# Kernel tuning notes

Measured on AMD Instinct MI355X. Metric: run time of the kernel, lower is better.

Reference implementation:

```python
import jax, jax.numpy as jnp
import numpy as np

N_CODEBOOKS = 4
N_EMBED = 1024
EMBED_DIM = 64
PATCH = 4
BETA = 0.25
EPS = 1e-5
USAGE_W = 0.01


def setup_inputs() -> dict:
    key = jax.random.key(0)
    k1, k2 = jax.random.split(key)
    z = jax.random.normal(k1, (8, 64, 128, 128), dtype=jnp.float32)
    # one EMA codebook per quantizer, initialized ~ randn like torch buffer
    codebooks = jax.random.normal(k2, (N_CODEBOOKS, N_EMBED, EMBED_DIM), dtype=jnp.float32)
    return {"z": z, "codebooks": codebooks}


def _usage_loss(indices, n_embed):
    # negative-entropy penalty on code usage (no gradient path: counts are ints)
    counts = jnp.bincount(indices.reshape(-1), length=n_embed).astype(jnp.float32)
    probs = (counts + EPS) / (counts.sum() + EPS * n_embed)
    entropy = -jnp.sum(probs * jnp.log(probs + EPS))
    return jnp.log(jnp.float32(n_embed)) - entropy


def _ema_quantize(residual, embedding):
    # residual: [N, C, ph, pw], embedding: [n_e, C]; eval mode (no EMA buffer update)
    N, C, ph, pw = residual.shape
    z_flat = residual.transpose(0, 2, 3, 1).reshape(-1, C)  # [M, C]
    d = (jnp.sum(z_flat ** 2, axis=1, keepdims=True)
         + jnp.sum(embedding ** 2, axis=1)
         - 2.0 * z_flat @ embedding.T)  # [M, n_e]
    idx = jnp.argmin(d, axis=1)  # [M]
    z_q = embedding[idx].reshape(N, ph, pw, C).transpose(0, 3, 1, 2)  # [N, C, ph, pw]
    loss = BETA * jnp.mean((jax.lax.stop_gradient(z_q) - residual) ** 2)
    z_q_st = residual + jax.lax.stop_gradient(z_q - residual)  # straight-through
    return z_q_st, loss, idx.reshape(N, ph, pw)


def reference(z, codebooks):
    B, C, H, W = z.shape
    h, w = H // PATCH, W // PATCH
    # b c (h ph) (w pw) -> (b h w) c ph pw
    zp = (z.reshape(B, C, h, PATCH, w, PATCH)
            .transpose(0, 2, 4, 1, 3, 5)
            .reshape(B * h * w, C, PATCH, PATCH))
    zq_acc = jnp.zeros_like(zp)
    residual = zp
    losses, all_idx = [], []
    for i in range(N_CODEBOOKS):
        zq_i, loss_i, idx_i = _ema_quantize(residual, codebooks[i])
        loss_i = loss_i + USAGE_W * _usage_loss(idx_i, N_EMBED)
        zq_acc = zq_acc + zq_i
        residual = residual - zq_i
        losses.append(loss_i)
        all_idx.append(idx_i.reshape(idx_i.shape[0], -1))  # [N, ph*pw]
    loss = jnp.stack(losses).sum()
    # (b h w) c ph pw -> b c (h ph) (w pw)
    z_q = (zq_acc.reshape(B, h, w, C, PATCH, PATCH)
                 .transpose(0, 3, 1, 4, 2, 5)
                 .reshape(B, C, H, W))
    # [N, patch_area, n_codebooks] -> [b, h, w, patch_area, n_codebooks]
    min_idx = jnp.stack(all_idx, axis=-1).reshape(B, h, w, PATCH * PATCH, N_CODEBOOKS)
    return z_q, loss, min_idx
```

## Files before the change

kernel.cpp:

```cpp
#include <hip/hip_runtime.h>
#include <math.h>

typedef __attribute__((ext_vector_type(8))) short short8;
typedef __attribute__((ext_vector_type(4))) float f32x4;

#define NCB 4
#define NE 1024
#define DIM 64
#define HW 16384
#define NPIX 131072
#define NWAVES 4096
#define MSE_DENOM 8388608.0f
#define EPSF 1e-5f
#define CHUNK_BYTES 24576
#define CHUNK_SHORTS 12288
#define NCHUNK 16

__device__ __forceinline__ unsigned short f2bf(float x) {
    unsigned u = __float_as_uint(x);
    u += 0x7fffu + ((u >> 16) & 1u);
    return (unsigned short)(u >> 16);
}
__device__ __forceinline__ float bf2f(unsigned short h) {
    return __uint_as_float(((unsigned)h) << 16);
}

__global__ __launch_bounds__(64) void rvq_norms(const float* __restrict__ cb,
                                                float* __restrict__ nrmh) {
    int code = blockIdx.x * 64 + threadIdx.x;
    const float4* row = reinterpret_cast<const float4*>(cb + (size_t)code * DIM);
    float s0 = 0.f, s1 = 0.f, s2 = 0.f, s3 = 0.f;
#pragma unroll
    for (int k = 0; k < 16; ++k) {
        float4 v = row[k];
        s0 = fmaf(v.x, v.x, s0); s1 = fmaf(v.y, v.y, s1);
        s2 = fmaf(v.z, v.z, s2); s3 = fmaf(v.w, v.w, s3);
    }
    nrmh[code] = -0.5f * ((s0 + s1) + (s2 + s3));
}

__global__ __launch_bounds__(256) void rvq_presplit(const float* __restrict__ cb,
                                                    unsigned short* __restrict__ gB) {
    int blk = blockIdx.x;
    int tid = threadIdx.x;
    int code = tid >> 2, dg = tid & 3;
    int c0 = (blk & 15) << 6;
    int i  = blk >> 4;
    const float4* s4 = reinterpret_cast<const float4*>(
        cb + ((size_t)i * NE + c0 + code) * DIM + dg * 16);
    float v[16];
    {
        float4 q;
        q = s4[0]; v[0]=q.x; v[1]=q.y; v[2]=q.z; v[3]=q.w;
        q = s4[1]; v[4]=q.x; v[5]=q.y; v[6]=q.z; v[7]=q.w;
        q = s4[2]; v[8]=q.x; v[9]=q.y; v[10]=q.z; v[11]=q.w;
        q = s4[3]; v[12]=q.x; v[13]=q.y; v[14]=q.z; v[15]=q.w;
    }
    char* outc = reinterpret_cast<char*>(gB + (size_t)blk * CHUNK_SHORTS);
    int linbase = code * 128 + dg * 32;
    int sw = (code & 7) << 4;
#pragma unroll
    for (int h = 0; h < 2; ++h) {
        short8 p1, p2, p3;
#pragma unroll
        for (int e = 0; e < 8; ++e) {
            float t = v[h * 8 + e];
            unsigned short u1 = f2bf(t); t -= bf2f(u1);
            unsigned short u2 = f2bf(t); t -= bf2f(u2);
            unsigned short u3 = f2bf(t);
            p1[e] = (short)u1; p2[e] = (short)u2; p3[e] = (short)u3;
        }
        int a = (linbase + h * 16) ^ sw;
        *reinterpret_cast<short8*>(outc + a)         = p1;
        *reinterpret_cast<short8*>(outc + 8192 + a)  = p2;
        *reinterpret_cast<short8*>(outc + 16384 + a) = p3;
    }
}

__device__ __forceinline__ void gload16(const void* gsrc, void* ldst) {
    __builtin_amdgcn_global_load_lds(
        (const __attribute__((address_space(1))) unsigned int*)gsrc,
        (__attribute__((address_space(3))) unsigned int*)ldst, 16, 0, 0);
}

__global__ __launch_bounds__(256, 2) void rvq_main(
    const float* __restrict__ z, const unsigned short* __restrict__ gB,
    const float* __restrict__ nrmh, const float* __restrict__ cb,
    float* __restrict__ out_zq, float* __restrict__ out_idx,
    unsigned* __restrict__ hist, float* __restrict__ msePartial)
{
    __shared__ uint4 sB[2][CHUNK_BYTES / 16];
    __shared__ int   sBest[4][32];

    const int tid  = threadIdx.x;
    const int lane = tid & 63;
    const int wid  = tid >> 6;
    const int col  = lane & 15;
    const int g    = lane >> 4;
    const int blockPix = blockIdx.x * 128;
    char* sBase = reinterpret_cast<char*>(sB);
    const int sw = (col & 7) << 4;

#pragma unroll
    for (int k = 0; k < 6; ++k)
        gload16(reinterpret_cast<const char*>(gB) + k * 4096 + tid * 16,
                sBase + k * 4096 + tid * 16);

    size_t zb[2];
#pragma unroll
    for (int m = 0; m < 2; ++m) {
        int pf = blockPix + wid * 32 + m * 16 + col;
        zb[m] = (size_t)(pf >> 14) * 1048576 + (size_t)(pf & 16383);
    }

    float r[2][2][8];
#pragma unroll
    for (int m = 0; m < 2; ++m)
#pragma unroll
        for (int kh = 0; kh < 2; ++kh)
#pragma unroll
            for (int e = 0; e < 8; ++e)
                r[m][kh][e] = z[zb[m] + (size_t)(kh * 32 + g * 8 + e) * HW];

    for (int i = 0; i < NCB; ++i) {
        const char* gBi = reinterpret_cast<const char*>(gB) + (size_t)i * NCHUNK * CHUNK_BYTES;
        const float* nrm_i = nrmh + i * NE;

        short8 A[3][2][2];
#pragma unroll
        for (int m = 0; m < 2; ++m)
#pragma unroll
            for (int kh = 0; kh < 2; ++kh)
#pragma unroll
                for (int e = 0; e < 8; ++e) {
                    float t = r[m][kh][e];
                    unsigned short u1 = f2bf(t); t -= bf2f(u1);
                    unsigned short u2 = f2bf(t); t -= bf2f(u2);
                    unsigned short u3 = f2bf(t);
                    A[0][m][kh][e] = (short)u1;
                    A[1][m][kh][e] = (short)u2;
                    A[2][m][kh][e] = (short)u3;
                }

        float maxv[2][4]; int maxi[2][4];
#pragma unroll
        for (int m = 0; m < 2; ++m)
#pragma unroll
            for (int rr = 0; rr < 4; ++rr) { maxv[m][rr] = -3.4e38f; maxi[m][rr] = 0; }

        for (int c = 0; c < NCHUNK; ++c) {
            __syncthreads();
            if (c < NCHUNK - 1) {
                const char* gc = gBi + (size_t)(c + 1) * CHUNK_BYTES;
                char* sbn = sBase + ((c + 1) & 1) * CHUNK_BYTES;
#pragma unroll
                for (int k = 0; k < 6; ++k)
                    gload16(gc + k * 4096 + tid * 16, sbn + k * 4096 + tid * 16);
            }
            const char* sbc = sBase + (c & 1) * CHUNK_BYTES;

#pragma unroll
            for (int sub = 0; sub < 4; ++sub) {
                const int code = (sub << 4) + col;
                float nh = nrm_i[(c << 6) + code];

                short8 B[3][2];
#pragma unroll
                for (int sb = 0; sb < 3; ++sb) {
                    B[sb][0] = *reinterpret_cast<const short8*>(
                        sbc + sb * 8192 + ((((code << 7) + (g << 4))) ^ sw));
                    B[sb][1] = *reinterpret_cast<const short8*>(
                        sbc + sb * 8192 + ((((code << 7) + 64 + (g << 4))) ^ sw));
                }

                f32x4 acc[2][3];
#pragma unroll
                for (int m = 0; m < 2; ++m)
#pragma unroll
                    for (int rr = 0; rr < 4; ++rr) {
                        acc[m][0][rr] = nh; acc[m][1][rr] = 0.f; acc[m][2][rr] = 0.f;
                    }

                __builtin_amdgcn_s_setprio(1);
#pragma unroll
                for (int sa = 0; sa < 3; ++sa) {
#pragma unroll
                    for (int kh = 0; kh < 2; ++kh)
#pragma unroll
                        for (int sb = 0; sb < 3 - sa; ++sb) {
                            acc[0][sb] = __builtin_amdgcn_mfma_f32_16x16x32_bf16(A[sa][0][kh], B[sb][kh], acc[0][sb], 0, 0, 0);
                            acc[1][sb] = __builtin_amdgcn_mfma_f32_16x16x32_bf16(A[sa][1][kh], B[sb][kh], acc[1][sb], 0, 0, 0);
                        }
                }
                __builtin_amdgcn_s_setprio(0);

#pragma unroll
                for (int m = 0; m < 2; ++m)
#pragma unroll
                    for (int rr = 0; rr < 4; ++rr) {
                        float s = (acc[m][0][rr] + acc[m][1][rr]) + acc[m][2][rr];
                        if (s > maxv[m][rr]) { maxv[m][rr] = s; maxi[m][rr] = (c << 6) + code; }
                    }
            }
        }

        if (i < NCB - 1) {
            const char* gn = reinterpret_cast<const char*>(gB)
                           + (size_t)(i + 1) * NCHUNK * CHUNK_BYTES;
#pragma unroll
            for (int k = 0; k < 6; ++k)
                gload16(gn + k * 4096 + tid * 16, sBase + k * 4096 + tid * 16);
        }

#pragma unroll
        for (int m = 0; m < 2; ++m)
#pragma unroll
            for (int rr = 0; rr < 4; ++rr) {
                float v = maxv[m][rr]; int ix = maxi[m][rr];
#pragma unroll
                for (int off = 1; off < 16; off <<= 1) {
                    float ov = __shfl_xor(v, off, 64);
                    int   oi = __shfl_xor(ix, off, 64);
                    if (ov > v || (ov == v && oi < ix)) { v = ov; ix = oi; }
                }
                maxi[m][rr] = ix;
            }
        if (col == 0) {
#pragma unroll
            for (int m = 0; m < 2; ++m)
#pragma unroll
                for (int rr = 0; rr < 4; ++rr)
                    sBest[wid][m * 16 + g * 4 + rr] = maxi[m][rr];
        }

        const float* cbi = cb + (size_t)i * NE * DIM;
        if (lane < 16) {
#pragma unroll
            for (int m = 0; m < 2; ++m) {
                int pfr = blockPix + wid * 32 + m * 16 + lane;
                int bb = pfr >> 14, yy = (pfr >> 7) & 127, xx = pfr & 127;
                int bi = sBest[wid][m * 16 + lane];
                size_t off = (size_t)bb * 65536 + (size_t)(yy >> 2) * 2048
                           + (size_t)(xx >> 2) * 64
                           + (size_t)(((yy & 3) << 2) + (xx & 3)) * 4 + (size_t)i;
                out_idx[off] = (float)bi;
                atomicAdd(&hist[i * NE + bi], 1u);
            }
        }

#pragma unroll
        for (int m = 0; m < 2; ++m) {
            const int best = sBest[wid][m * 16 + col];
            const float* er = cbi + (size_t)best * DIM;
#pragma unroll
            for (int kh = 0; kh < 2; ++kh) {
                const float4* e4 = reinterpret_cast<const float4*>(er + kh * 32 + g * 8);
                float4 q0 = e4[0], q1 = e4[1];
                r[m][kh][0] -= q0.x; r[m][kh][1] -= q0.y;
                r[m][kh][2] -= q0.z; r[m][kh][3] -= q0.w;
                r[m][kh][4] -= q1.x; r[m][kh][5] -= q1.y;
                r[m][kh][6] -= q1.z; r[m][kh][7] -= q1.w;
            }
        }

        float s = 0.f;
#pragma unroll
        for (int m = 0; m < 2; ++m)
#pragma unroll
            for (int kh = 0; kh < 2; ++kh)
#pragma unroll
                for (int e = 0; e < 8; ++e) s = fmaf(r[m][kh][e], r[m][kh][e], s);
#pragma unroll
        for (int d_ = 32; d_ > 0; d_ >>= 1) s += __shfl_down(s, d_, 64);
        if (lane == 0) msePartial[i * NWAVES + blockIdx.x * 4 + wid] = s;
    }

#pragma unroll
    for (int m = 0; m < 2; ++m)
#pragma unroll
        for (int kh = 0; kh < 2; ++kh)
#pragma unroll
            for (int e = 0; e < 8; ++e) {
                size_t o = zb[m] + (size_t)(kh * 32 + g * 8 + e) * HW;
                out_zq[o] = z[o] - r[m][kh][e];
            }
}

__global__ __launch_bounds__(1024) void rvq_finalize(
    const unsigned* __restrict__ hist, const float* __restrict__ msePartial,
    float* __restrict__ out_loss)
{
    __shared__ float red[1024];
    int t = threadIdx.x;
    float loss = 0.f;
    for (int i = 0; i < NCB; ++i) {
        float cnt = (float)hist[i * NE + t];
        float prob = (cnt + EPSF) / (131072.0f + EPSF * 1024.0f);
        red[t] = -prob * logf(prob + EPSF);
        __syncthreads();
        for (int s = 512; s > 0; s >>= 1) { if (t < s) red[t] += red[t + s]; __syncthreads(); }
        float entropy = red[0];
        __syncthreads();
        float acc = 0.f;
#pragma unroll
        for (int k = 0; k < 4; ++k) acc += msePartial[i * NWAVES + k * 1024 + t];
        red[t] = acc;
        __syncthreads();
        for (int s = 512; s > 0; s >>= 1) { if (t < s) red[t] += red[t + s]; __syncthreads(); }
        float mse_sum = red[0];
        __syncthreads();
        loss += 0.25f * (mse_sum / MSE_DENOM) + 0.01f * (logf(1024.0f) - entropy);
    }
    if (t == 0) out_loss[0] = loss;
}

extern "C" void kernel_launch(void* const* d_in, const int* in_sizes, int n_in,
                              void* d_out, int out_size, void* d_ws, size_t ws_size,
                              hipStream_t stream) {
    const float* z  = (const float*)d_in[0];
    const float* cb = (const float*)d_in[1];

    float* out      = (float*)d_out;
    float* out_zq   = out;
    float* out_loss = out + 8388608;
    float* out_idx  = out + 8388609;

    unsigned* hist        = (unsigned*)d_ws;
    float*    nrmh        = (float*)((char*)d_ws + 16384);
    float*    msePartial  = (float*)((char*)d_ws + 32768);
    unsigned short* gB    = (unsigned short*)((char*)d_ws + 163840);

    hipMemsetAsync(d_ws, 0, 16384, stream);
    rvq_norms<<<64, 64, 0, stream>>>(cb, nrmh);
    rvq_presplit<<<64, 256, 0, stream>>>(cb, gB);
    rvq_main<<<1024, 256, 0, stream>>>(z, gB, nrmh, cb, out_zq, out_idx, hist, msePartial);
    rvq_finalize<<<1, 1024, 0, stream>>>(hist, msePartial, out_loss);
}
```

Baseline: 435.0 us.

## Prefilter codes with single-bf16 pass, rescore candidates at full precision

Nearest-code search becomes two stages. A cheap single-bf16 MFMA pass finds each pixel's approximate max score, then a bound from the residual and codebook norms sets a threshold. A second bf16 pass pushes codes above that threshold into a per-wave shared-memory list, and only those candidates are rescored with the 3-way split-bf16 product. This removes most of the 6-MFMA-per-tile exact work but adds a second sweep over the codebook, ballot and atomic list building, and uncached global gathers during rescoring. Correctness depends on the error bound and on the candidate list not overflowing CAP.

```diff
diff --git a/kernel.cpp b/kernel.cpp
--- a/kernel.cpp
+++ b/kernel.cpp
@@ -12,9 +12,9 @@
 #define NWAVES 4096
 #define MSE_DENOM 8388608.0f
 #define EPSF 1e-5f
-#define CHUNK_BYTES 24576
-#define CHUNK_SHORTS 12288
-#define NCHUNK 16
+#define CH1_BYTES 16384
+#define NCH1 8
+#define CAP 1024
 
 __device__ __forceinline__ unsigned short f2bf(float x) {
     unsigned u = __float_as_uint(x);
@@ -26,7 +26,8 @@
 }
 
 __global__ __launch_bounds__(64) void rvq_norms(const float* __restrict__ cb,
-                                                float* __restrict__ nrmh) {
+                                                float* __restrict__ nrmh,
+                                                float* __restrict__ emax2) {
     int code = blockIdx.x * 64 + threadIdx.x;
     const float4* row = reinterpret_cast<const float4*>(cb + (size_t)code * DIM);
     float s0 = 0.f, s1 = 0.f, s2 = 0.f, s3 = 0.f;
@@ -36,18 +37,22 @@
         s0 = fmaf(v.x, v.x, s0); s1 = fmaf(v.y, v.y, s1);
         s2 = fmaf(v.z, v.z, s2); s3 = fmaf(v.w, v.w, s3);
     }
-    nrmh[code] = -0.5f * ((s0 + s1) + (s2 + s3));
+    float n2 = (s0 + s1) + (s2 + s3);
+    nrmh[code] = -0.5f * n2;
+    atomicMax((int*)&emax2[blockIdx.x >> 4], __float_as_int(n2));
 }
 
 __global__ __launch_bounds__(256) void rvq_presplit(const float* __restrict__ cb,
-                                                    unsigned short* __restrict__ gB) {
+                                                    unsigned short* __restrict__ gB1,
+                                                    unsigned short* __restrict__ gBf) {
     int blk = blockIdx.x;
     int tid = threadIdx.x;
-    int code = tid >> 2, dg = tid & 3;
+    int code64 = tid >> 2, dg = tid & 3;
     int c0 = (blk & 15) << 6;
     int i  = blk >> 4;
+    int C  = c0 + code64;
     const float4* s4 = reinterpret_cast<const float4*>(
-        cb + ((size_t)i * NE + c0 + code) * DIM + dg * 16);
+        cb + ((size_t)i * NE + C) * DIM + dg * 16);
     float v[16];
     {
         float4 q;
@@ -56,9 +61,9 @@
         q = s4[2]; v[8]=q.x; v[9]=q.y; v[10]=q.z; v[11]=q.w;
         q = s4[3]; v[12]=q.x; v[13]=q.y; v[14]=q.z; v[15]=q.w;
     }
-    char* outc = reinterpret_cast<char*>(gB + (size_t)blk * CHUNK_SHORTS);
-    int linbase = code * 128 + dg * 32;
-    int sw = (code & 7) << 4;
+    char* out1 = reinterpret_cast<char*>(gB1) + (size_t)i * 131072 + (size_t)C * 128;
+    char* outf = reinterpret_cast<char*>(gBf) + (size_t)i * 393216 + (size_t)C * 384;
+    int sw = (C & 7) << 4;
 #pragma unroll
     for (int h = 0; h < 2; ++h) {
         short8 p1, p2, p3;
@@ -70,10 +75,11 @@
             unsigned short u3 = f2bf(t);
             p1[e] = (short)u1; p2[e] = (short)u2; p3[e] = (short)u3;
         }
-        int a = (linbase + h * 16) ^ sw;
-        *reinterpret_cast<short8*>(outc + a)         = p1;
-        *reinterpret_cast<short8*>(outc + 8192 + a)  = p2;
-        *reinterpret_cast<short8*>(outc + 16384 + a) = p3;
+        int al = dg * 32 + h * 16;
+        *reinterpret_cast<short8*>(out1 + (al ^ sw)) = p1;
+        *reinterpret_cast<short8*>(outf + al)        = p1;
+        *reinterpret_cast<short8*>(outf + 128 + al)  = p2;
+        *reinterpret_cast<short8*>(outf + 256 + al)  = p3;
     }
 }
 
@@ -84,13 +90,18 @@
 }
 
 __global__ __launch_bounds__(256, 2) void rvq_main(
-    const float* __restrict__ z, const unsigned short* __restrict__ gB,
-    const float* __restrict__ nrmh, const float* __restrict__ cb,
+    const float* __restrict__ z, const unsigned short* __restrict__ gB1,
+    const unsigned short* __restrict__ gBf,
+    const float* __restrict__ nrmh, const float* __restrict__ emax2,
+    const float* __restrict__ cb,
     float* __restrict__ out_zq, float* __restrict__ out_idx,
     unsigned* __restrict__ hist, float* __restrict__ msePartial)
 {
-    __shared__ uint4 sB[2][CHUNK_BYTES / 16];
+    __shared__ uint4 sB[2][CH1_BYTES / 16];
     __shared__ int   sBest[4][32];
+    __shared__ float sRn[4][32];
+    __shared__ int   sList[4][CAP];
+    __shared__ int   sCnt[4];
 
     const int tid  = threadIdx.x;
     const int lane = tid & 63;
@@ -100,11 +111,12 @@
     const int blockPix = blockIdx.x * 128;
     char* sBase = reinterpret_cast<char*>(sB);
     const int sw = (col & 7) << 4;
-
-#pragma unroll
-    for (int k = 0; k < 6; ++k)
-        gload16(reinterpret_cast<const char*>(gB) + k * 4096 + tid * 16,
-                sBase + k * 4096 + tid * 16);
+    const char* gB1b = reinterpret_cast<const char*>(gB1);
+    const char* gBfb = reinterpret_cast<const char*>(gBf);
+
+#pragma unroll
+    for (int k = 0; k < 4; ++k)
+        gload16(gB1b + k * 4096 + tid * 16, sBase + k * 4096 + tid * 16);
 
     size_t zb[2];
 #pragma unroll
@@ -123,17 +135,22 @@
                 r[m][kh][e] = z[zb[m] + (size_t)(kh * 32 + g * 8 + e) * HW];
 
     for (int i = 0; i < NCB; ++i) {
-        const char* gBi = reinterpret_cast<const char*>(gB) + (size_t)i * NCHUNK * CHUNK_BYTES;
+        const char* gB1i = gB1b + (size_t)i * 131072;
+        const char* gBfi = gBfb + (size_t)i * 393216;
         const float* nrm_i = nrmh + i * NE;
+        if (lane == 0) sCnt[wid] = 0;
 
         short8 A[3][2][2];
+        float rn2[2] = {0.f, 0.f};
 #pragma unroll
         for (int m = 0; m < 2; ++m)
 #pragma unroll
             for (int kh = 0; kh < 2; ++kh)
 #pragma unroll
                 for (int e = 0; e < 8; ++e) {
-                    float t = r[m][kh][e];
+                    float t0 = r[m][kh][e];
+                    rn2[m] = fmaf(t0, t0, rn2[m]);
+                    float t = t0;
                     unsigned short u1 = f2bf(t); t -= bf2f(u1);
                     unsigned short u2 = f2bf(t); t -= bf2f(u2);
                     unsigned short u3 = f2bf(t);
@@ -141,96 +158,194 @@
                     A[1][m][kh][e] = (short)u2;
                     A[2][m][kh][e] = (short)u3;
                 }
-
-        float maxv[2][4]; int maxi[2][4];
-#pragma unroll
-        for (int m = 0; m < 2; ++m)
-#pragma unroll
-            for (int rr = 0; rr < 4; ++rr) { maxv[m][rr] = -3.4e38f; maxi[m][rr] = 0; }
-
-        for (int c = 0; c < NCHUNK; ++c) {
+#pragma unroll
+        for (int m = 0; m < 2; ++m) {
+            rn2[m] += __shfl_xor(rn2[m], 16, 64);
+            rn2[m] += __shfl_xor(rn2[m], 32, 64);
+        }
+        if (lane < 16) { sRn[wid][lane] = rn2[0]; sRn[wid][16 + lane] = rn2[1]; }
+
+        float maxv[2][4];
+#pragma unroll
+        for (int m = 0; m < 2; ++m)
+#pragma unroll
+            for (int rr = 0; rr < 4; ++rr) maxv[m][rr] = -3.4e38f;
+
+        for (int c = 0; c < NCH1; ++c) {
             __syncthreads();
-            if (c < NCHUNK - 1) {
-                const char* gc = gBi + (size_t)(c + 1) * CHUNK_BYTES;
-                char* sbn = sBase + ((c + 1) & 1) * CHUNK_BYTES;
-#pragma unroll
-                for (int k = 0; k < 6; ++k)
+            {
+                int nc = (c < NCH1 - 1) ? c + 1 : 0;
+                const char* gc = gB1i + (size_t)nc * CH1_BYTES;
+                char* sbn = sBase + ((c + 1) & 1) * CH1_BYTES;
+#pragma unroll
+                for (int k = 0; k < 4; ++k)
                     gload16(gc + k * 4096 + tid * 16, sbn + k * 4096 + tid * 16);
             }
-            const char* sbc = sBase + (c & 1) * CHUNK_BYTES;
-
-#pragma unroll
-            for (int sub = 0; sub < 4; ++sub) {
+            const char* sbc = sBase + (c & 1) * CH1_BYTES;
+#pragma unroll
+            for (int sub = 0; sub < 8; ++sub) {
                 const int code = (sub << 4) + col;
-                float nh = nrm_i[(c << 6) + code];
-
-                short8 B[3][2];
-#pragma unroll
-                for (int sb = 0; sb < 3; ++sb) {
-                    B[sb][0] = *reinterpret_cast<const short8*>(
-                        sbc + sb * 8192 + ((((code << 7) + (g << 4))) ^ sw));
-                    B[sb][1] = *reinterpret_cast<const short8*>(
-                        sbc + sb * 8192 + ((((code << 7) + 64 + (g << 4))) ^ sw));
-                }
-
-                f32x4 acc[2][3];
-#pragma unroll
-                for (int m = 0; m < 2; ++m)
-#pragma unroll
-                    for (int rr = 0; rr < 4; ++rr) {
-                        acc[m][0][rr] = nh; acc[m][1][rr] = 0.f; acc[m][2][rr] = 0.f;
+                float nh = nrm_i[(c << 7) + code];
+                short8 B0 = *reinterpret_cast<const short8*>(
+                    sbc + ((((code << 7) + (g << 4))) ^ sw));
+                short8 B1 = *reinterpret_cast<const short8*>(
+                    sbc + ((((code << 7) + 64 + (g << 4))) ^ sw));
+                f32x4 acc0, acc1;
+#pragma unroll
+                for (int rr = 0; rr < 4; ++rr) { acc0[rr] = nh; acc1[rr] = nh; }
+                __builtin_amdgcn_s_setprio(1);
+                acc0 = __builtin_amdgcn_mfma_f32_16x16x32_bf16(A[0][0][0], B0, acc0, 0, 0, 0);
+                acc1 = __builtin_amdgcn_mfma_f32_16x16x32_bf16(A[0][1][0], B0, acc1, 0, 0, 0);
+                acc0 = __builtin_amdgcn_mfma_f32_16x16x32_bf16(A[0][0][1], B1, acc0, 0, 0, 0);
+                acc1 = __builtin_amdgcn_mfma_f32_16x16x32_bf16(A[0][1][1], B1, acc1, 0, 0, 0);
+                __builtin_amdgcn_s_setprio(0);
+#pragma unroll
+                for (int rr = 0; rr < 4; ++rr) {
+                    maxv[0][rr] = fmaxf(maxv[0][rr], acc0[rr]);
+                    maxv[1][rr] = fmaxf(maxv[1][rr], acc1[rr]);
+                }
+            }
+        }
+
+#pragma unroll
+        for (int m = 0; m < 2; ++m)
+#pragma unroll
+            for (int rr = 0; rr < 4; ++rr) {
+#pragma unroll
+                for (int off = 1; off < 16; off <<= 1)
+                    maxv[m][rr] = fmaxf(maxv[m][rr], __shfl_xor(maxv[m][rr], off, 64));
+            }
+
+        float thr[2][4];
+        {
+            float en = sqrtf(emax2[i]);
+#pragma unroll
+            for (int m = 0; m < 2; ++m)
+#pragma unroll
+                for (int rr = 0; rr < 4; ++rr) {
+                    float rn = sqrtf(sRn[wid][m * 16 + g * 4 + rr]);
+                    thr[m][rr] = maxv[m][rr] - (0.0205f * rn * en + 8e-3f);
+                }
+        }
+
+        for (int c = 0; c < NCH1; ++c) {
+            __syncthreads();
+            if (c < NCH1 - 1) {
+                const char* gc = gB1i + (size_t)(c + 1) * CH1_BYTES;
+                char* sbn = sBase + ((c + 1) & 1) * CH1_BYTES;
+#pragma unroll
+                for (int k = 0; k < 4; ++k)
+                    gload16(gc + k * 4096 + tid * 16, sbn + k * 4096 + tid * 16);
+            }
+            const char* sbc = sBase + (c & 1) * CH1_BYTES;
+#pragma unroll
+            for (int sub = 0; sub < 8; ++sub) {
+                const int code = (sub << 4) + col;
+                float nh = nrm_i[(c << 7) + code];
+                short8 B0 = *reinterpret_cast<const short8*>(
+                    sbc + ((((code << 7) + (g << 4))) ^ sw));
+                short8 B1 = *reinterpret_cast<const short8*>(
+                    sbc + ((((code << 7) + 64 + (g << 4))) ^ sw));
+                f32x4 acc0, acc1;
+#pragma unroll
+                for (int rr = 0; rr < 4; ++rr) { acc0[rr] = nh; acc1[rr] = nh; }
+                __builtin_amdgcn_s_setprio(1);
+                acc0 = __builtin_amdgcn_mfma_f32_16x16x32_bf16(A[0][0][0], B0, acc0, 0, 0, 0);
+                acc1 = __builtin_amdgcn_mfma_f32_16x16x32_bf16(A[0][1][0], B0, acc1, 0, 0, 0);
+                acc0 = __builtin_amdgcn_mfma_f32_16x16x32_bf16(A[0][0][1], B1, acc0, 0, 0, 0);
+                acc1 = __builtin_amdgcn_mfma_f32_16x16x32_bf16(A[0][1][1], B1, acc1, 0, 0, 0);
+                __builtin_amdgcn_s_setprio(0);
+                bool anyhit = false;
+#pragma unroll
+                for (int rr = 0; rr < 4; ++rr) {
+                    anyhit |= (acc0[rr] >= thr[0][rr]);
+                    anyhit |= (acc1[rr] >= thr[1][rr]);
+                }
+                unsigned long long mb = __ballot(anyhit);
+                if (mb) {
+                    unsigned long long colmask = 0x0001000100010001ULL << col;
+                    bool push = anyhit &&
+                        !(mb & colmask & ((lane == 0) ? 0ULL : ((1ULL << lane) - 1)));
+                    if (push) {
+                        int p = atomicAdd(&sCnt[wid], 1);
+                        if (p < CAP) sList[wid][p] = (c << 7) + code;
                     }
-
-                __builtin_amdgcn_s_setprio(1);
-#pragma unroll
-                for (int sa = 0; sa < 3; ++sa) {
-#pragma unroll
-                    for (int kh = 0; kh < 2; ++kh)
-#pragma unroll
-                        for (int sb = 0; sb < 3 - sa; ++sb) {
-                            acc[0][sb] = __builtin_amdgcn_mfma_f32_16x16x32_bf16(A[sa][0][kh], B[sb][kh], acc[0][sb], 0, 0, 0);
-                            acc[1][sb] = __builtin_amdgcn_mfma_f32_16x16x32_bf16(A[sa][1][kh], B[sb][kh], acc[1][sb], 0, 0, 0);
-                        }
-                }
-                __builtin_amdgcn_s_setprio(0);
-
-#pragma unroll
-                for (int m = 0; m < 2; ++m)
-#pragma unroll
-                    for (int rr = 0; rr < 4; ++rr) {
-                        float s = (acc[m][0][rr] + acc[m][1][rr]) + acc[m][2][rr];
-                        if (s > maxv[m][rr]) { maxv[m][rr] = s; maxi[m][rr] = (c << 6) + code; }
-                    }
+                }
             }
         }
 
         if (i < NCB - 1) {
-            const char* gn = reinterpret_cast<const char*>(gB)
-                           + (size_t)(i + 1) * NCHUNK * CHUNK_BYTES;
-#pragma unroll
-            for (int k = 0; k < 6; ++k)
+            const char* gn = gB1b + (size_t)(i + 1) * 131072;
+#pragma unroll
+            for (int k = 0; k < 4; ++k)
                 gload16(gn + k * 4096 + tid * 16, sBase + k * 4096 + tid * 16);
         }
 
-#pragma unroll
-        for (int m = 0; m < 2; ++m)
+        float bestv[2][4]; int besti[2][4];
+#pragma unroll
+        for (int m = 0; m < 2; ++m)
+#pragma unroll
+            for (int rr = 0; rr < 4; ++rr) { bestv[m][rr] = -3.4e38f; besti[m][rr] = 0x7fffffff; }
+
+        int ncand = sCnt[wid]; if (ncand > CAP) ncand = CAP;
+        for (int b = 0; b < ncand; b += 16) {
+            int ci = b + col;
+            int code = sList[wid][ci < ncand ? ci : 0];
+            const char* base = gBfi + (size_t)code * 384;
+            short8 B[3][2];
+#pragma unroll
+            for (int s = 0; s < 3; ++s) {
+                B[s][0] = *reinterpret_cast<const short8*>(base + s * 128 + (g << 4));
+                B[s][1] = *reinterpret_cast<const short8*>(base + s * 128 + 64 + (g << 4));
+            }
+            float nh = nrm_i[code];
+            f32x4 acc0, acc1;
+#pragma unroll
+            for (int rr = 0; rr < 4; ++rr) { acc0[rr] = nh; acc1[rr] = nh; }
+            __builtin_amdgcn_s_setprio(1);
+#pragma unroll
+            for (int sb = 0; sb < 3; ++sb) {
+#pragma unroll
+                for (int sa = 0; sa < 3 - sb; ++sa) {
+                    acc0 = __builtin_amdgcn_mfma_f32_16x16x32_bf16(A[sa][0][0], B[sb][0], acc0, 0, 0, 0);
+                    acc1 = __builtin_amdgcn_mfma_f32_16x16x32_bf16(A[sa][1][0], B[sb][0], acc1, 0, 0, 0);
+                    acc0 = __builtin_amdgcn_mfma_f32_16x16x32_bf16(A[sa][0][1], B[sb][1], acc0, 0, 0, 0);
+                    acc1 = __builtin_amdgcn_mfma_f32_16x16x32_bf16(A[sa][1][1], B[sb][1], acc1, 0, 0, 0);
+                }
+            }
+            __builtin_amdgcn_s_setprio(0);
 #pragma unroll
             for (int rr = 0; rr < 4; ++rr) {
-                float v = maxv[m][rr]; int ix = maxi[m][rr];
+                float s0 = acc0[rr];
+                if (s0 > bestv[0][rr] || (s0 == bestv[0][rr] && code < besti[0][rr])) {
+                    bestv[0][rr] = s0; besti[0][rr] = code;
+                }
+                float s1 = acc1[rr];
+                if (s1 > bestv[1][rr] || (s1 == bestv[1][rr] && code < besti[1][rr])) {
+                    bestv[1][rr] = s1; besti[1][rr] = code;
+                }
+            }
+        }
+
+#pragma unroll
+        for (int m = 0; m < 2; ++m)
+#pragma unroll
+            for (int rr = 0; rr < 4; ++rr) {
+                float v = bestv[m][rr]; int ix = besti[m][rr];
 #pragma unroll
                 for (int off = 1; off < 16; off <<= 1) {
                     float ov = __shfl_xor(v, off, 64);
                     int   oi = __shfl_xor(ix, off, 64);
                     if (ov > v || (ov == v && oi < ix)) { v = ov; ix = oi; }
                 }
-                maxi[m][rr] = ix;
+                besti[m][rr] = ix;
             }
         if (col == 0) {
 #pragma unroll
             for (int m = 0; m < 2; ++m)
 #pragma unroll
                 for (int rr = 0; rr < 4; ++rr)
-                    sBest[wid][m * 16 + g * 4 + rr] = maxi[m][rr];
+                    sBest[wid][m * 16 + g * 4 + rr] = besti[m][rr];
         }
 
         const float* cbi = cb + (size_t)i * NE * DIM;
@@ -326,13 +441,16 @@
     float* out_idx  = out + 8388609;
 
     unsigned* hist        = (unsigned*)d_ws;
-    float*    nrmh        = (float*)((char*)d_ws + 16384);
-    float*    msePartial  = (float*)((char*)d_ws + 32768);
-    unsigned short* gB    = (unsigned short*)((char*)d_ws + 163840);
-
-    hipMemsetAsync(d_ws, 0, 16384, stream);
-    rvq_norms<<<64, 64, 0, stream>>>(cb, nrmh);
-    rvq_presplit<<<64, 256, 0, stream>>>(cb, gB);
-    rvq_main<<<1024, 256, 0, stream>>>(z, gB, nrmh, cb, out_zq, out_idx, hist, msePartial);
+    float*    emax2       = (float*)((char*)d_ws + 16384);
+    float*    nrmh        = (float*)((char*)d_ws + 32768);
+    float*    msePartial  = (float*)((char*)d_ws + 49152);
+    unsigned short* gB1   = (unsigned short*)((char*)d_ws + 131072);
+    unsigned short* gBf   = (unsigned short*)((char*)d_ws + 655360);
+
+    hipMemsetAsync(d_ws, 0, 16448, stream);
+    rvq_norms<<<64, 64, 0, stream>>>(cb, nrmh, emax2);
+    rvq_presplit<<<64, 256, 0, stream>>>(cb, gB1, gBf);
+    rvq_main<<<1024, 256, 0, stream>>>(z, gB1, gBf, nrmh, emax2, cb,
+                                       out_zq, out_idx, hist, msePartial);
     rvq_finalize<<<1, 1024, 0, stream>>>(hist, msePartial, out_loss);
 }
```

Result: no change. 430.7 us (-1.0%).
